# Performance work log

Measured on AMD Instinct MI355X. Metric: run time of the kernel, lower is better.

The kernel has to match this reference:

```python
import jax, jax.numpy as jnp
import numpy as np

HIDDEN = 1024
FFN = 2048
NUM_EXPERTS = 16
JITTER_EPS = 0.01


def setup_inputs() -> dict:
    key = jax.random.key(0)
    k1, k2, k3, k4 = jax.random.split(key, 4)
    hidden_states = jax.random.normal(k1, (4, 2048, HIDDEN), dtype=jnp.float32)
    gate_weight = jax.random.normal(k2, (NUM_EXPERTS, HIDDEN), dtype=jnp.float32) * 0.02
    # gate_up_weights[e, :FFN] = w1 (gate proj), [FFN:] = w3 (up proj)
    gate_up_weights = jax.random.normal(k3, (NUM_EXPERTS, 2 * FFN, HIDDEN), dtype=jnp.float32) * 0.02
    down_weights = jax.random.normal(k4, (NUM_EXPERTS, HIDDEN, FFN), dtype=jnp.float32) * 0.02
    return {
        'hidden_states': hidden_states,
        'gate_weight': gate_weight,
        'gate_up_weights': gate_up_weights,
        'down_weights': down_weights,
    }


def sparsemixer(scores, jitter_eps):
    # top-1 selection with jitter mask
    m1 = jnp.max(scores, axis=-1, keepdims=True)              # [T,1]
    ind1 = jnp.argmax(scores, axis=-1, keepdims=True)         # [T,1]
    factor1 = jnp.maximum(jnp.abs(scores), m1)
    mask1 = (m1 - scores) / factor1 > 2.0 * jitter_eps
    gates1 = jax.nn.softmax(jnp.where(mask1, -jnp.inf, scores), axis=-1)
    w1 = jnp.take_along_axis(gates1, ind1, axis=-1)           # [T,1]

    # mask out top-1, select top-2
    top1_onehot = jax.nn.one_hot(ind1[:, 0], scores.shape[-1], dtype=bool)
    masked_scores = jnp.where(top1_onehot, -jnp.inf, scores)
    m2 = jnp.max(masked_scores, axis=-1, keepdims=True)
    ind2 = jnp.argmax(masked_scores, axis=-1, keepdims=True)
    factor2 = jnp.maximum(jnp.abs(scores), m2)
    mask2 = (m2 - scores) / factor2 > 2.0 * jitter_eps
    gates2 = jax.nn.softmax(jnp.where(mask2, -jnp.inf, masked_scores), axis=-1)
    w2 = jnp.take_along_axis(gates2, ind2, axis=-1)           # [T,1]

    multipliers = jnp.concatenate([w1, w2], axis=-1)          # [T,2]
    experts = jnp.concatenate([ind1, ind2], axis=-1)          # [T,2] int
    return multipliers, experts


def fused_moe(x, gate_up_weights, down_weights, routing_weights, selected_experts):
    # x: [T,H], gate_up: [E,2F,H], down: [E,H,F]
    E = gate_up_weights.shape[0]
    ffn = down_weights.shape[2]
    # combine[t,e] = sum_k routing_weights[t,k] * (selected[t,k]==e)
    onehot = jax.nn.one_hot(selected_experts, E, dtype=x.dtype)     # [T,2,E]
    combine = jnp.einsum('tk,tke->te', routing_weights, onehot)     # [T,E]
    out = jnp.zeros_like(x)
    for e in range(E):
        gu = x @ gate_up_weights[e].T                                # [T,2F]
        h = jax.nn.silu(gu[:, :ffn]) * gu[:, ffn:]                   # [T,F]
        out = out + combine[:, e:e + 1] * (h @ down_weights[e].T)    # [T,H]
    return out


def reference(hidden_states, gate_weight, gate_up_weights, down_weights):
    B, S, H = hidden_states.shape
    x = hidden_states.reshape(-1, H)                         # [T,H]
    router_logits = x @ gate_weight.T                        # [T,E]
    routing_weights, selected_experts = sparsemixer(router_logits, JITTER_EPS)
    out = fused_moe(x, gate_up_weights, down_weights, routing_weights, selected_experts)
    return out.reshape(B, S, H), router_logits
```

## Files before the change

kernel.cpp:

```cpp
#include <hip/hip_runtime.h>
#include <hip/hip_bf16.h>
#include <math.h>

#define T_TOKENS 8192
#define HID 1024
#define FFN 2048
#define NEXP 16
#define NPAIR (2*T_TOKENS)
#define TM 128
#define MAXTILES 144

typedef short bf16x8 __attribute__((ext_vector_type(8)));
typedef float f32x4 __attribute__((ext_vector_type(4)));

static const size_t HPACK_OFF = 0;
static const size_t HPACK_SZ  = (size_t)MAXTILES * 32 * 16384;
static const size_t GPACK_OFF = HPACK_OFF + HPACK_SZ;
static const size_t GPACK_SZ  = (size_t)16 * 64 * 16 * 8192;
static const size_t DPACK_OFF = GPACK_OFF + GPACK_SZ;
static const size_t DPACK_SZ  = (size_t)16 * 16 * 32 * 8192;
static const size_t APACK_OFF = DPACK_OFF + DPACK_SZ;
static const size_t APACK_SZ  = (size_t)MAXTILES * 16 * 16384;
static const size_t WTK_OFF   = APACK_OFF + APACK_SZ;
static const size_t ETK_OFF   = WTK_OFF  + (size_t)NPAIR*4;
static const size_t RANK_OFF  = ETK_OFF  + (size_t)NPAIR*4;
static const size_t LIST_OFF  = RANK_OFF + (size_t)NPAIR*4;
static const size_t CNT_OFF   = LIST_OFF + (size_t)NPAIR*4;
static const size_t OFFS_OFF  = CNT_OFF  + 64;
static const size_t TEXP_OFF  = OFFS_OFF + 128;
static const size_t TSEG_OFF  = TEXP_OFF + (size_t)MAXTILES*4;
static const size_t HDR_OFF   = TSEG_OFF + (size_t)MAXTILES*4;

__device__ __forceinline__ unsigned short f2bf(float f) {
  union { float f; unsigned u; } v; v.f = f;
  unsigned r = v.u + 0x7fff + ((v.u >> 16) & 1);
  return (unsigned short)(r >> 16);
}

__device__ __forceinline__ bf16x8 pack8(float4 a, float4 b) {
  bf16x8 r;
  r[0]=(short)f2bf(a.x); r[1]=(short)f2bf(a.y); r[2]=(short)f2bf(a.z); r[3]=(short)f2bf(a.w);
  r[4]=(short)f2bf(b.x); r[5]=(short)f2bf(b.y); r[6]=(short)f2bf(b.z); r[7]=(short)f2bf(b.w);
  return r;
}

__device__ __forceinline__ void ld16(const unsigned short* g, unsigned short* l) {
  __builtin_amdgcn_global_load_lds((const __attribute__((address_space(1))) void*)g,
                                   (__attribute__((address_space(3))) void*)l, 16, 0, 0);
}

__global__ __launch_bounds__(256) void k_pack(const float* __restrict__ src, unsigned short* __restrict__ dst,
                                              int nbcnt, int kbcnt, int kdim) {
  int e = blockIdx.z, nb = blockIdx.y, kb = blockIdx.x;
  __shared__ unsigned short tile[4096];
  int tid = threadIdx.x;
  int n = tid >> 2, ks = (tid & 3) * 16;
  const float* s = src + ((size_t)((e*nbcnt + nb)*64 + n))*kdim + kb*64 + ks;
  float4 f0 = *(const float4*)(s);
  float4 f1 = *(const float4*)(s + 4);
  float4 f2 = *(const float4*)(s + 8);
  float4 f3 = *(const float4*)(s + 12);
  int kkc0 = ks >> 3;
  *(bf16x8*)&tile[(kkc0*64 + n)*8]     = pack8(f0, f1);
  *(bf16x8*)&tile[((kkc0+1)*64 + n)*8] = pack8(f2, f3);
  __syncthreads();
  unsigned short* d = dst + ((size_t)(e*nbcnt + nb)*kbcnt + kb)*4096 + tid*16;
  *(bf16x8*)(d)     = *(const bf16x8*)&tile[tid*16];
  *(bf16x8*)(d + 8) = *(const bf16x8*)&tile[tid*16 + 8];
}

__global__ __launch_bounds__(256) void k_logits(const float* __restrict__ x,
                                                const float* __restrict__ gw,
                                                float* __restrict__ logits) {
  int tid = threadIdx.x;
  int wave = tid >> 6, lane = tid & 63;
  int t = blockIdx.x * 4 + wave;
  const float* xp = x + (size_t)t * HID;
  float acc[NEXP];
  #pragma unroll
  for (int e = 0; e < NEXP; e++) acc[e] = 0.f;
  for (int i = lane; i < HID; i += 64) {
    float xv = xp[i];
    #pragma unroll
    for (int e = 0; e < NEXP; e++) acc[e] += xv * gw[e*HID + i];
  }
  float mine = 0.f;
  #pragma unroll
  for (int e = 0; e < NEXP; e++) {
    float v = acc[e];
    #pragma unroll
    for (int o = 32; o > 0; o >>= 1) v += __shfl_xor(v, o, 64);
    if (lane == e) mine = v;
  }
  if (lane < NEXP) logits[(size_t)t*NEXP + lane] = mine;
}

__global__ __launch_bounds__(256) void k_route(const float* __restrict__ logits,
                                               float* __restrict__ wtk, int* __restrict__ etk,
                                               int* __restrict__ rank, int* __restrict__ counts) {
  int t = blockIdx.x*256 + threadIdx.x;
  if (t >= T_TOKENS) return;
  float s[NEXP];
  const float* lp = logits + (size_t)t*NEXP;
  #pragma unroll
  for (int e = 0; e < NEXP; e++) s[e] = lp[e];

  float m1 = s[0]; int i1 = 0;
  #pragma unroll
  for (int e = 1; e < NEXP; e++) if (s[e] > m1) { m1 = s[e]; i1 = e; }
  float sum1 = 0.f;
  #pragma unroll
  for (int e = 0; e < NEXP; e++) {
    float f = fmaxf(fabsf(s[e]), m1);
    if (!((m1 - s[e]) > 0.02f*f)) sum1 += expf(s[e]-m1);
  }
  float m2 = -INFINITY; int i2 = 0;
  #pragma unroll
  for (int e = 0; e < NEXP; e++) if (e != i1 && s[e] > m2) { m2 = s[e]; i2 = e; }
  float sum2 = 0.f;
  #pragma unroll
  for (int e = 0; e < NEXP; e++) {
    if (e == i1) continue;
    float f = fmaxf(fabsf(s[e]), m2);
    if (!((m2 - s[e]) > 0.02f*f)) sum2 += expf(s[e]-m2);
  }
  wtk[t*2]   = 1.f/sum1;
  wtk[t*2+1] = 1.f/sum2;
  etk[t*2]   = i1;
  etk[t*2+1] = i2;
  rank[t*2]   = atomicAdd(&counts[i1], 1);
  rank[t*2+1] = atomicAdd(&counts[i2], 1);
}

__global__ void k_scan(const int* __restrict__ counts, int* __restrict__ offsets,
                       int* __restrict__ texp, int* __restrict__ tseg, int* __restrict__ hdr) {
  if (threadIdx.x != 0 || blockIdx.x != 0) return;
  int off = 0, nt = 0;
  for (int e = 0; e < NEXP; e++) {
    offsets[e] = off;
    int c = counts[e];
    int tiles = (c + TM - 1)/TM;
    for (int i = 0; i < tiles; i++) { texp[nt] = e; tseg[nt] = i; nt++; }
    off += c;
  }
  offsets[NEXP] = off;
  hdr[0] = nt;
}

__global__ __launch_bounds__(256) void k_scatter(const int* __restrict__ etk,
                                                 const int* __restrict__ rank,
                                                 const int* __restrict__ offsets,
                                                 int* __restrict__ list) {
  int p = blockIdx.x*256 + threadIdx.x;
  if (p >= NPAIR) return;
  int e = etk[p];
  list[offsets[e] + rank[p]] = p;
}

__global__ __launch_bounds__(256) void k_agather(const float* __restrict__ x,
                                                 const int* __restrict__ list,
                                                 const int* __restrict__ counts,
                                                 const int* __restrict__ offsets,
                                                 const int* __restrict__ texp,
                                                 const int* __restrict__ tseg,
                                                 const int* __restrict__ hdr,
                                                 unsigned short* __restrict__ apack) {
  int by = blockIdx.x;
  if (by >= hdr[0]) return;
  int e = texp[by];
  int m0 = tseg[by]*TM;
  int seg0 = offsets[e];
  int cnt = counts[e];
  __shared__ int toks[TM];
  int tid = threadIdx.x;
  if (tid < TM) toks[tid] = list[seg0 + min(m0 + tid, cnt-1)] >> 1;
  __syncthreads();
  #pragma unroll 4
  for (int it = 0; it < 64; ++it) {
    int flat = it*256 + tid;
    int kb = flat >> 10;
    int i  = flat & 1023;
    int kkc = i >> 7, row = i & 127;
    const float* s = x + (size_t)toks[row]*HID + kb*64 + kkc*8;
    float4 f0 = *(const float4*)(s);
    float4 f1 = *(const float4*)(s + 4);
    *(bf16x8*)(apack + ((size_t)(by*16 + kb))*8192 + (size_t)i*8) = pack8(f0, f1);
  }
}

__global__ __launch_bounds__(256,4) void k_gateup(const unsigned short* __restrict__ apack,
                                                  const unsigned short* __restrict__ gpack,
                                                  const float* __restrict__ wtk,
                                                  const int* __restrict__ list,
                                                  const int* __restrict__ counts,
                                                  const int* __restrict__ offsets,
                                                  const int* __restrict__ texp,
                                                  const int* __restrict__ tseg,
                                                  const int* __restrict__ hdr,
                                                  unsigned short* __restrict__ hpack) {
  int fb = blockIdx.x;
  int by = blockIdx.y;
  if (by >= hdr[0]) return;
  int e = texp[by];
  int m0 = tseg[by]*TM;
  int seg0 = offsets[e];
  int cnt = counts[e];
  int rows = min(TM, cnt - m0);

  __shared__ __align__(16) unsigned short A_lds[8192];
  __shared__ __align__(16) unsigned short Bg_lds[4096];
  __shared__ __align__(16) unsigned short Bu_lds[4096];

  int tid = threadIdx.x;
  int wid = tid >> 6, lane = tid & 63;
  int wr = wid >> 1, wc = wid & 1;
  int c4 = lane >> 4, r16 = lane & 15;

  const unsigned short* gA = apack + (size_t)by * 16 * 8192;
  const unsigned short* gG = gpack + (size_t)(e*64 + fb)      * 16 * 4096;
  const unsigned short* gU = gpack + (size_t)(e*64 + 32 + fb) * 16 * 4096;

  f32x4 accg[4][2] = {};
  f32x4 accu[4][2] = {};

  for (int kb = 0; kb < 16; ++kb) {
    #pragma unroll
    for (int s = 0; s < 8; ++s) {
      int i = wid*8 + s;
      if (i < 16) {
        ld16(gA + (size_t)kb*8192 + i*512 + lane*8, &A_lds[i*512]);
      } else if (i < 24) {
        int j = i - 16;
        ld16(gG + (size_t)kb*4096 + j*512 + lane*8, &Bg_lds[j*512]);
      } else {
        int j = i - 24;
        ld16(gU + (size_t)kb*4096 + j*512 + lane*8, &Bu_lds[j*512]);
      }
    }
    __syncthreads();
    #pragma unroll
    for (int kk = 0; kk < 2; ++kk) {
      bf16x8 a[4], bg[2], bu[2];
      #pragma unroll
      for (int sm = 0; sm < 4; ++sm)
        a[sm] = *(const bf16x8*)&A_lds[((kk*4 + c4)*128 + wr*64 + sm*16 + r16)*8];
      #pragma unroll
      for (int sn = 0; sn < 2; ++sn) {
        bg[sn] = *(const bf16x8*)&Bg_lds[((kk*4 + c4)*64 + wc*32 + sn*16 + r16)*8];
        bu[sn] = *(const bf16x8*)&Bu_lds[((kk*4 + c4)*64 + wc*32 + sn*16 + r16)*8];
      }
      #pragma unroll
      for (int sm = 0; sm < 4; ++sm)
        #pragma unroll
        for (int sn = 0; sn < 2; ++sn) {
          accg[sm][sn] = __builtin_amdgcn_mfma_f32_16x16x32_bf16(a[sm], bg[sn], accg[sm][sn], 0, 0, 0);
          accu[sm][sn] = __builtin_amdgcn_mfma_f32_16x16x32_bf16(a[sm], bu[sn], accu[sm][sn], 0, 0, 0);
        }
    }
    __syncthreads();
  }

  #pragma unroll
  for (int sm = 0; sm < 4; ++sm) {
    #pragma unroll
    for (int j = 0; j < 4; ++j) {
      int row = wr*64 + sm*16 + (lane>>4)*4 + j;
      float w = (row < rows) ? wtk[list[seg0 + m0 + row]] : 0.f;
      #pragma unroll
      for (int sn = 0; sn < 2; ++sn) {
        int col = wc*32 + sn*16 + (lane & 15);
        float g = accg[sm][sn][j];
        float u = accu[sm][sn][j];
        float hv = g / (1.f + __expf(-g)) * u * w;
        A_lds[((col>>3)*128 + row)*8 + (col&7)] = f2bf(hv);
      }
    }
  }
  __syncthreads();
  unsigned short* dst = hpack + ((size_t)(by*32 + fb))*8192 + tid*32;
  const unsigned short* srcl = &A_lds[tid*32];
  #pragma unroll
  for (int q = 0; q < 4; ++q)
    *(bf16x8*)(dst + q*8) = *(const bf16x8*)(srcl + q*8);
}

__global__ __launch_bounds__(256,4) void k_down(const unsigned short* __restrict__ hpack,
                                                const unsigned short* __restrict__ dpack,
                                                const int* __restrict__ list,
                                                const int* __restrict__ counts,
                                                const int* __restrict__ offsets,
                                                const int* __restrict__ texp,
                                                const int* __restrict__ tseg,
                                                const int* __restrict__ hdr,
                                                float* __restrict__ out) {
  int nb = blockIdx.x;
  int by = blockIdx.y;
  if (by >= hdr[0]) return;
  int e = texp[by];
  int m0 = tseg[by]*TM;
  int seg0 = offsets[e];
  int cnt = counts[e];
  int rows = min(TM, cnt - m0);

  __shared__ __align__(16) unsigned short A_lds[8192];
  __shared__ __align__(16) unsigned short B_lds[8192];

  int tid = threadIdx.x;
  int wid = tid >> 6, lane = tid & 63;
  int wr = wid >> 1, wc = wid & 1;
  int c4 = lane >> 4, r16 = lane & 15;

  const unsigned short* hA = hpack + (size_t)by * 32 * 8192;

  f32x4 acc[4][4] = {};

  for (int kb = 0; kb < 32; ++kb) {
    #pragma unroll
    for (int s = 0; s < 8; ++s) {
      int i = wid*8 + s;
      if (i < 16) {
        ld16(hA + (size_t)kb*8192 + i*512 + lane*8, &A_lds[i*512]);
      } else {
        int i2 = i - 16;
        int p = i2 >> 3, j = i2 & 7;
        ld16(dpack + (((size_t)(e*16 + nb*2 + p))*32 + kb)*4096 + j*512 + lane*8,
             &B_lds[p*4096 + j*512]);
      }
    }
    __syncthreads();
    #pragma unroll
    for (int kk = 0; kk < 2; ++kk) {
      bf16x8 a[4], b[4];
      #pragma unroll
      for (int sm = 0; sm < 4; ++sm)
        a[sm] = *(const bf16x8*)&A_lds[((kk*4 + c4)*128 + wr*64 + sm*16 + r16)*8];
      #pragma unroll
      for (int sn = 0; sn < 4; ++sn) {
        int col = wc*64 + sn*16 + r16;
        b[sn] = *(const bf16x8*)&B_lds[(col>>6)*4096 + ((kk*4 + c4)*64 + (col & 63))*8];
      }
      #pragma unroll
      for (int sm = 0; sm < 4; ++sm)
        #pragma unroll
        for (int sn = 0; sn < 4; ++sn)
          acc[sm][sn] = __builtin_amdgcn_mfma_f32_16x16x32_bf16(a[sm], b[sn], acc[sm][sn], 0, 0, 0);
    }
    __syncthreads();
  }

  #pragma unroll
  for (int sm = 0; sm < 4; ++sm) {
    #pragma unroll
    for (int j = 0; j < 4; ++j) {
      int row = wr*64 + sm*16 + (lane>>4)*4 + j;
      if (row < rows) {
        int t = list[seg0 + m0 + row] >> 1;
        #pragma unroll
        for (int sn = 0; sn < 4; ++sn) {
          int col = nb*128 + wc*64 + sn*16 + r16;
          unsafeAtomicAdd(&out[(size_t)t*HID + col], acc[sm][sn][j]);
        }
      }
    }
  }
}

extern "C" void kernel_launch(void* const* d_in, const int* in_sizes, int n_in,
                              void* d_out, int out_size, void* d_ws, size_t ws_size,
                              hipStream_t stream) {
  const float* x   = (const float*)d_in[0];
  const float* gw  = (const float*)d_in[1];
  const float* gup = (const float*)d_in[2];
  const float* dwn = (const float*)d_in[3];

  float* out = (float*)d_out;
  float* logits = out + (size_t)T_TOKENS*HID;

  char* ws = (char*)d_ws;
  unsigned short* hpack = (unsigned short*)(ws + HPACK_OFF);
  unsigned short* gpack = (unsigned short*)(ws + GPACK_OFF);
  unsigned short* dpack = (unsigned short*)(ws + DPACK_OFF);
  unsigned short* apack = (unsigned short*)(ws + APACK_OFF);
  float* wtk   = (float*)(ws + WTK_OFF);
  int* etk     = (int*)(ws + ETK_OFF);
  int* rank    = (int*)(ws + RANK_OFF);
  int* list    = (int*)(ws + LIST_OFF);
  int* counts  = (int*)(ws + CNT_OFF);
  int* offsets = (int*)(ws + OFFS_OFF);
  int* texp    = (int*)(ws + TEXP_OFF);
  int* tseg    = (int*)(ws + TSEG_OFF);
  int* hdr     = (int*)(ws + HDR_OFF);

  hipMemsetAsync(out, 0, (size_t)T_TOKENS*HID*4, stream);
  hipMemsetAsync(counts, 0, 64, stream);

  k_logits<<<T_TOKENS/4, 256, 0, stream>>>(x, gw, logits);
  k_route<<<T_TOKENS/256, 256, 0, stream>>>(logits, wtk, etk, rank, counts);
  k_scan<<<1, 64, 0, stream>>>(counts, offsets, texp, tseg, hdr);
  k_scatter<<<NPAIR/256, 256, 0, stream>>>(etk, rank, offsets, list);
  k_agather<<<MAXTILES, 256, 0, stream>>>(x, list, counts, offsets, texp, tseg, hdr, apack);

  {
    dim3 g(16, 64, NEXP);
    k_pack<<<g, 256, 0, stream>>>(gup, gpack, 64, 16, HID);
  }
  {
    dim3 g(32, 16, NEXP);
    k_pack<<<g, 256, 0, stream>>>(dwn, dpack, 16, 32, FFN);
  }

  dim3 g3(32, MAXTILES);
  k_gateup<<<g3, 256, 0, stream>>>(apack, gpack, wtk, list, counts, offsets, texp, tseg, hdr, hpack);

  dim3 g4(8, MAXTILES);
  k_down<<<g4, 256, 0, stream>>>(hpack, dpack, list, counts, offsets, texp, tseg, hdr, out);
}
```

Measured before the change: 569.5 us.

## Double-buffer LDS in expert GEMMs and replace atomic scatter with slot buffer plus combine

The gate-up and down GEMM kernels now load half-size K tiles into ping-pong LDS buffers, so the global-to-LDS copy for the next step is issued before the MFMAs on the current one. The down kernel no longer atomically adds into the output. It writes each routed row into a per-slot buffer that reuses the gpack workspace region, and a new k_final kernel sums each token's two slots into the output, which also removes the output memset. This trades atomics and the memset for one extra kernel launch and an extra write-then-read of a 64 MB intermediate.

```diff
diff --git a/kernel.cpp b/kernel.cpp
--- a/kernel.cpp
+++ b/kernel.cpp
@@ -207,59 +207,70 @@
   int cnt = counts[e];
   int rows = min(TM, cnt - m0);
 
-  __shared__ __align__(16) unsigned short A_lds[8192];
-  __shared__ __align__(16) unsigned short Bg_lds[4096];
-  __shared__ __align__(16) unsigned short Bu_lds[4096];
+  __shared__ __align__(16) unsigned short A_lds[2][4096];
+  __shared__ __align__(16) unsigned short Bg_lds[2][2048];
+  __shared__ __align__(16) unsigned short Bu_lds[2][2048];
 
   int tid = threadIdx.x;
   int wid = tid >> 6, lane = tid & 63;
   int wr = wid >> 1, wc = wid & 1;
   int c4 = lane >> 4, r16 = lane & 15;
 
-  const unsigned short* gA = apack + (size_t)by * 16 * 8192;
-  const unsigned short* gG = gpack + (size_t)(e*64 + fb)      * 16 * 4096;
-  const unsigned short* gU = gpack + (size_t)(e*64 + 32 + fb) * 16 * 4096;
+  const unsigned short* gA = apack + (size_t)by * 131072;
+  const unsigned short* gG = gpack + ((size_t)(e*64 + fb))      * 65536;
+  const unsigned short* gU = gpack + ((size_t)(e*64 + 32 + fb)) * 65536;
 
   f32x4 accg[4][2] = {};
   f32x4 accu[4][2] = {};
 
-  for (int kb = 0; kb < 16; ++kb) {
-    #pragma unroll
-    for (int s = 0; s < 8; ++s) {
-      int i = wid*8 + s;
-      if (i < 16) {
-        ld16(gA + (size_t)kb*8192 + i*512 + lane*8, &A_lds[i*512]);
-      } else if (i < 24) {
-        int j = i - 16;
-        ld16(gG + (size_t)kb*4096 + j*512 + lane*8, &Bg_lds[j*512]);
+  auto STAGE = [&](int buf, int kb) {
+    #pragma unroll
+    for (int s = 0; s < 4; ++s) {
+      int i = wid*4 + s;
+      if (i < 8) {
+        ld16(gA + (size_t)kb*4096 + i*512 + lane*8, &A_lds[buf][i*512]);
+      } else if (i < 12) {
+        int j = i - 8;
+        ld16(gG + (size_t)kb*2048 + j*512 + lane*8, &Bg_lds[buf][j*512]);
       } else {
-        int j = i - 24;
-        ld16(gU + (size_t)kb*4096 + j*512 + lane*8, &Bu_lds[j*512]);
+        int j = i - 12;
+        ld16(gU + (size_t)kb*2048 + j*512 + lane*8, &Bu_lds[buf][j*512]);
       }
     }
-    __syncthreads();
-    #pragma unroll
-    for (int kk = 0; kk < 2; ++kk) {
-      bf16x8 a[4], bg[2], bu[2];
-      #pragma unroll
-      for (int sm = 0; sm < 4; ++sm)
-        a[sm] = *(const bf16x8*)&A_lds[((kk*4 + c4)*128 + wr*64 + sm*16 + r16)*8];
+  };
+
+  auto COMPUTE = [&](int buf) {
+    bf16x8 a[4], bg[2], bu[2];
+    #pragma unroll
+    for (int sm = 0; sm < 4; ++sm)
+      a[sm] = *(const bf16x8*)&A_lds[buf][(c4*128 + wr*64 + sm*16 + r16)*8];
+    #pragma unroll
+    for (int sn = 0; sn < 2; ++sn) {
+      bg[sn] = *(const bf16x8*)&Bg_lds[buf][(c4*64 + wc*32 + sn*16 + r16)*8];
+      bu[sn] = *(const bf16x8*)&Bu_lds[buf][(c4*64 + wc*32 + sn*16 + r16)*8];
+    }
+    #pragma unroll
+    for (int sm = 0; sm < 4; ++sm)
       #pragma unroll
       for (int sn = 0; sn < 2; ++sn) {
-        bg[sn] = *(const bf16x8*)&Bg_lds[((kk*4 + c4)*64 + wc*32 + sn*16 + r16)*8];
-        bu[sn] = *(const bf16x8*)&Bu_lds[((kk*4 + c4)*64 + wc*32 + sn*16 + r16)*8];
+        accg[sm][sn] = __builtin_amdgcn_mfma_f32_16x16x32_bf16(a[sm], bg[sn], accg[sm][sn], 0, 0, 0);
+        accu[sm][sn] = __builtin_amdgcn_mfma_f32_16x16x32_bf16(a[sm], bu[sn], accu[sm][sn], 0, 0, 0);
       }
-      #pragma unroll
-      for (int sm = 0; sm < 4; ++sm)
-        #pragma unroll
-        for (int sn = 0; sn < 2; ++sn) {
-          accg[sm][sn] = __builtin_amdgcn_mfma_f32_16x16x32_bf16(a[sm], bg[sn], accg[sm][sn], 0, 0, 0);
-          accu[sm][sn] = __builtin_amdgcn_mfma_f32_16x16x32_bf16(a[sm], bu[sn], accu[sm][sn], 0, 0, 0);
-        }
-    }
+  };
+
+  STAGE(0, 0);
+  __syncthreads();
+  int cur = 0;
+  for (int kb = 0; kb < 31; ++kb) {
+    STAGE(cur ^ 1, kb + 1);
+    COMPUTE(cur);
     __syncthreads();
-  }
-
+    cur ^= 1;
+  }
+  COMPUTE(cur);
+  __syncthreads();
+
+  unsigned short* scr = &A_lds[0][0];
   #pragma unroll
   for (int sm = 0; sm < 4; ++sm) {
     #pragma unroll
@@ -272,13 +283,13 @@
         float g = accg[sm][sn][j];
         float u = accu[sm][sn][j];
         float hv = g / (1.f + __expf(-g)) * u * w;
-        A_lds[((col>>3)*128 + row)*8 + (col&7)] = f2bf(hv);
+        scr[((col>>3)*128 + row)*8 + (col&7)] = f2bf(hv);
       }
     }
   }
   __syncthreads();
   unsigned short* dst = hpack + ((size_t)(by*32 + fb))*8192 + tid*32;
-  const unsigned short* srcl = &A_lds[tid*32];
+  const unsigned short* srcl = scr + tid*32;
   #pragma unroll
   for (int q = 0; q < 4; ++q)
     *(bf16x8*)(dst + q*8) = *(const bf16x8*)(srcl + q*8);
@@ -286,13 +297,12 @@
 
 __global__ __launch_bounds__(256,4) void k_down(const unsigned short* __restrict__ hpack,
                                                 const unsigned short* __restrict__ dpack,
-                                                const int* __restrict__ list,
                                                 const int* __restrict__ counts,
-                                                const int* __restrict__ offsets,
                                                 const int* __restrict__ texp,
                                                 const int* __restrict__ tseg,
+                                                const int* __restrict__ offsets,
                                                 const int* __restrict__ hdr,
-                                                float* __restrict__ out) {
+                                                float* __restrict__ ydown) {
   int nb = blockIdx.x;
   int by = blockIdx.y;
   if (by >= hdr[0]) return;
@@ -302,51 +312,60 @@
   int cnt = counts[e];
   int rows = min(TM, cnt - m0);
 
-  __shared__ __align__(16) unsigned short A_lds[8192];
-  __shared__ __align__(16) unsigned short B_lds[8192];
+  __shared__ __align__(16) unsigned short A_lds[2][4096];
+  __shared__ __align__(16) unsigned short B_lds[2][4096];
 
   int tid = threadIdx.x;
   int wid = tid >> 6, lane = tid & 63;
   int wr = wid >> 1, wc = wid & 1;
   int c4 = lane >> 4, r16 = lane & 15;
 
-  const unsigned short* hA = hpack + (size_t)by * 32 * 8192;
+  const unsigned short* hA = hpack + (size_t)by * 262144;
 
   f32x4 acc[4][4] = {};
 
-  for (int kb = 0; kb < 32; ++kb) {
-    #pragma unroll
-    for (int s = 0; s < 8; ++s) {
-      int i = wid*8 + s;
-      if (i < 16) {
-        ld16(hA + (size_t)kb*8192 + i*512 + lane*8, &A_lds[i*512]);
+  auto STAGE = [&](int buf, int kb) {
+    #pragma unroll
+    for (int s = 0; s < 4; ++s) {
+      int i = wid*4 + s;
+      if (i < 8) {
+        ld16(hA + (size_t)kb*4096 + i*512 + lane*8, &A_lds[buf][i*512]);
       } else {
-        int i2 = i - 16;
-        int p = i2 >> 3, j = i2 & 7;
-        ld16(dpack + (((size_t)(e*16 + nb*2 + p))*32 + kb)*4096 + j*512 + lane*8,
-             &B_lds[p*4096 + j*512]);
+        int i2 = i - 8;
+        int p = i2 >> 2, j = i2 & 3;
+        ld16(dpack + (((size_t)(e*16 + nb*2 + p))*32 + (kb>>1))*4096 + (kb&1)*2048 + j*512 + lane*8,
+             &B_lds[buf][p*2048 + j*512]);
       }
     }
+  };
+
+  auto COMPUTE = [&](int buf) {
+    bf16x8 a[4], b[4];
+    #pragma unroll
+    for (int sm = 0; sm < 4; ++sm)
+      a[sm] = *(const bf16x8*)&A_lds[buf][(c4*128 + wr*64 + sm*16 + r16)*8];
+    #pragma unroll
+    for (int sn = 0; sn < 4; ++sn) {
+      int col = wc*64 + sn*16 + r16;
+      b[sn] = *(const bf16x8*)&B_lds[buf][(col>>6)*2048 + (c4*64 + (col&63))*8];
+    }
+    #pragma unroll
+    for (int sm = 0; sm < 4; ++sm)
+      #pragma unroll
+      for (int sn = 0; sn < 4; ++sn)
+        acc[sm][sn] = __builtin_amdgcn_mfma_f32_16x16x32_bf16(a[sm], b[sn], acc[sm][sn], 0, 0, 0);
+  };
+
+  STAGE(0, 0);
+  __syncthreads();
+  int cur = 0;
+  for (int kb = 0; kb < 63; ++kb) {
+    STAGE(cur ^ 1, kb + 1);
+    COMPUTE(cur);
     __syncthreads();
-    #pragma unroll
-    for (int kk = 0; kk < 2; ++kk) {
-      bf16x8 a[4], b[4];
-      #pragma unroll
-      for (int sm = 0; sm < 4; ++sm)
-        a[sm] = *(const bf16x8*)&A_lds[((kk*4 + c4)*128 + wr*64 + sm*16 + r16)*8];
-      #pragma unroll
-      for (int sn = 0; sn < 4; ++sn) {
-        int col = wc*64 + sn*16 + r16;
-        b[sn] = *(const bf16x8*)&B_lds[(col>>6)*4096 + ((kk*4 + c4)*64 + (col & 63))*8];
-      }
-      #pragma unroll
-      for (int sm = 0; sm < 4; ++sm)
-        #pragma unroll
-        for (int sn = 0; sn < 4; ++sn)
-          acc[sm][sn] = __builtin_amdgcn_mfma_f32_16x16x32_bf16(a[sm], b[sn], acc[sm][sn], 0, 0, 0);
-    }
-    __syncthreads();
-  }
+    cur ^= 1;
+  }
+  COMPUTE(cur);
 
   #pragma unroll
   for (int sm = 0; sm < 4; ++sm) {
@@ -354,15 +373,31 @@
     for (int j = 0; j < 4; ++j) {
       int row = wr*64 + sm*16 + (lane>>4)*4 + j;
       if (row < rows) {
-        int t = list[seg0 + m0 + row] >> 1;
+        size_t slot = (size_t)(seg0 + m0 + row);
         #pragma unroll
         for (int sn = 0; sn < 4; ++sn) {
           int col = nb*128 + wc*64 + sn*16 + r16;
-          unsafeAtomicAdd(&out[(size_t)t*HID + col], acc[sm][sn][j]);
+          ydown[slot*HID + col] = acc[sm][sn][j];
         }
       }
     }
   }
+}
+
+__global__ __launch_bounds__(256) void k_final(const float* __restrict__ ydown,
+                                               const int* __restrict__ etk,
+                                               const int* __restrict__ rank,
+                                               const int* __restrict__ offsets,
+                                               float* __restrict__ out) {
+  int t = blockIdx.x;
+  int c = threadIdx.x;
+  int p0 = t*2, p1 = t*2 + 1;
+  int s0 = offsets[etk[p0]] + rank[p0];
+  int s1 = offsets[etk[p1]] + rank[p1];
+  float4 a = *(const float4*)(ydown + (size_t)s0*HID + c*4);
+  float4 b = *(const float4*)(ydown + (size_t)s1*HID + c*4);
+  float4 r; r.x = a.x+b.x; r.y = a.y+b.y; r.z = a.z+b.z; r.w = a.w+b.w;
+  *(float4*)(out + (size_t)t*HID + c*4) = r;
 }
 
 extern "C" void kernel_launch(void* const* d_in, const int* in_sizes, int n_in,
@@ -381,6 +416,7 @@
   unsigned short* gpack = (unsigned short*)(ws + GPACK_OFF);
   unsigned short* dpack = (unsigned short*)(ws + DPACK_OFF);
   unsigned short* apack = (unsigned short*)(ws + APACK_OFF);
+  float* ydown = (float*)(ws + GPACK_OFF);
   float* wtk   = (float*)(ws + WTK_OFF);
   int* etk     = (int*)(ws + ETK_OFF);
   int* rank    = (int*)(ws + RANK_OFF);
@@ -391,7 +427,6 @@
   int* tseg    = (int*)(ws + TSEG_OFF);
   int* hdr     = (int*)(ws + HDR_OFF);
 
-  hipMemsetAsync(out, 0, (size_t)T_TOKENS*HID*4, stream);
   hipMemsetAsync(counts, 0, 64, stream);
 
   k_logits<<<T_TOKENS/4, 256, 0, stream>>>(x, gw, logits);
@@ -413,5 +448,7 @@
   k_gateup<<<g3, 256, 0, stream>>>(apack, gpack, wtk, list, counts, offsets, texp, tseg, hdr, hpack);
 
   dim3 g4(8, MAXTILES);
-  k_down<<<g4, 256, 0, stream>>>(hpack, dpack, list, counts, offsets, texp, tseg, hdr, out);
-}
+  k_down<<<g4, 256, 0, stream>>>(hpack, dpack, counts, texp, tseg, offsets, hdr, ydown);
+
+  k_final<<<T_TOKENS, 256, 0, stream>>>(ydown, etk, rank, offsets, out);
+}
```

Result: no change. 562.8 us (-1.2%).

## Merge pack kernels into gather/gate-up launches and replace atomics with slot-ordered reduction

Applied to the files above, without the earlier changes.

The gate-up weight pack now runs inside the token-gather launch, and the down-weight pack runs as extra blocks of the gate-up launch, which cuts the launch count and lets the packing overlap with other work. The down projection no longer does atomic adds into a zeroed output. It writes each pair's result to a per-slot buffer that reuses the gate-pack workspace, and a new final kernel sums the two expert contributions per token. This removes the output memset and the atomic contention, at the cost of an extra 64MB write and read. Reusing gpack space for ydown is only safe because gate-up has finished by the time down runs.

```diff
diff --git a/kernel.cpp b/kernel.cpp
--- a/kernel.cpp
+++ b/kernel.cpp
@@ -49,10 +49,9 @@
                                    (__attribute__((address_space(3))) void*)l, 16, 0, 0);
 }
 
-__global__ __launch_bounds__(256) void k_pack(const float* __restrict__ src, unsigned short* __restrict__ dst,
-                                              int nbcnt, int kbcnt, int kdim) {
-  int e = blockIdx.z, nb = blockIdx.y, kb = blockIdx.x;
-  __shared__ unsigned short tile[4096];
+__device__ __forceinline__ void pack_body(const float* __restrict__ src, unsigned short* __restrict__ dst,
+                                          int e, int nb, int kb, int nbcnt, int kbcnt, int kdim,
+                                          unsigned short* tile ) {
   int tid = threadIdx.x;
   int n = tid >> 2, ks = (tid & 3) * 16;
   const float* s = src + ((size_t)((e*nbcnt + nb)*64 + n))*kdim + kb*64 + ks;
@@ -157,21 +156,30 @@
   list[offsets[e] + rank[p]] = p;
 }
 
-__global__ __launch_bounds__(256) void k_agather(const float* __restrict__ x,
-                                                 const int* __restrict__ list,
-                                                 const int* __restrict__ counts,
-                                                 const int* __restrict__ offsets,
-                                                 const int* __restrict__ texp,
-                                                 const int* __restrict__ tseg,
-                                                 const int* __restrict__ hdr,
-                                                 unsigned short* __restrict__ apack) {
-  int by = blockIdx.x;
+__global__ __launch_bounds__(256) void k_prep(const float* __restrict__ gup,
+                                              unsigned short* __restrict__ gpack,
+                                              const float* __restrict__ x,
+                                              const int* __restrict__ list,
+                                              const int* __restrict__ counts,
+                                              const int* __restrict__ offsets,
+                                              const int* __restrict__ texp,
+                                              const int* __restrict__ tseg,
+                                              const int* __restrict__ hdr,
+                                              unsigned short* __restrict__ apack) {
+  __shared__ __align__(16) unsigned short tile[4096];
+  int bid = blockIdx.x;
+  if (bid < 16384) {
+    int kb = bid & 15, nb = (bid >> 4) & 63, e = bid >> 10;
+    pack_body(gup, gpack, e, nb, kb, 64, 16, HID, tile);
+    return;
+  }
+  int by = bid - 16384;
   if (by >= hdr[0]) return;
   int e = texp[by];
   int m0 = tseg[by]*TM;
   int seg0 = offsets[e];
   int cnt = counts[e];
-  __shared__ int toks[TM];
+  int* toks = (int*)tile;
   int tid = threadIdx.x;
   if (tid < TM) toks[tid] = list[seg0 + min(m0 + tid, cnt-1)] >> 1;
   __syncthreads();
@@ -190,6 +198,8 @@
 
 __global__ __launch_bounds__(256,4) void k_gateup(const unsigned short* __restrict__ apack,
                                                   const unsigned short* __restrict__ gpack,
+                                                  const float* __restrict__ dwn,
+                                                  unsigned short* __restrict__ dpack,
                                                   const float* __restrict__ wtk,
                                                   const int* __restrict__ list,
                                                   const int* __restrict__ counts,
@@ -198,8 +208,15 @@
                                                   const int* __restrict__ tseg,
                                                   const int* __restrict__ hdr,
                                                   unsigned short* __restrict__ hpack) {
-  int fb = blockIdx.x;
-  int by = blockIdx.y;
+  __shared__ __align__(16) unsigned short lds[16384];
+  int bid = blockIdx.x;
+  if (bid >= 4608) {
+    int p = bid - 4608;
+    pack_body(dwn, dpack, p >> 9, (p >> 5) & 15, p & 31, 16, 32, FFN, lds);
+    return;
+  }
+  int fb = bid & 31;
+  int by = bid >> 5;
   if (by >= hdr[0]) return;
   int e = texp[by];
   int m0 = tseg[by]*TM;
@@ -207,18 +224,18 @@
   int cnt = counts[e];
   int rows = min(TM, cnt - m0);
 
-  __shared__ __align__(16) unsigned short A_lds[8192];
-  __shared__ __align__(16) unsigned short Bg_lds[4096];
-  __shared__ __align__(16) unsigned short Bu_lds[4096];
+  unsigned short* A_lds  = lds;
+  unsigned short* Bg_lds = lds + 8192;
+  unsigned short* Bu_lds = lds + 12288;
 
   int tid = threadIdx.x;
   int wid = tid >> 6, lane = tid & 63;
   int wr = wid >> 1, wc = wid & 1;
   int c4 = lane >> 4, r16 = lane & 15;
 
-  const unsigned short* gA = apack + (size_t)by * 16 * 8192;
-  const unsigned short* gG = gpack + (size_t)(e*64 + fb)      * 16 * 4096;
-  const unsigned short* gU = gpack + (size_t)(e*64 + 32 + fb) * 16 * 4096;
+  const unsigned short* gA = apack + (size_t)by * 131072;
+  const unsigned short* gG = gpack + (size_t)(e*64 + fb)      * 65536;
+  const unsigned short* gU = gpack + (size_t)(e*64 + 32 + fb) * 65536;
 
   f32x4 accg[4][2] = {};
   f32x4 accu[4][2] = {};
@@ -286,13 +303,12 @@
 
 __global__ __launch_bounds__(256,4) void k_down(const unsigned short* __restrict__ hpack,
                                                 const unsigned short* __restrict__ dpack,
-                                                const int* __restrict__ list,
                                                 const int* __restrict__ counts,
-                                                const int* __restrict__ offsets,
                                                 const int* __restrict__ texp,
                                                 const int* __restrict__ tseg,
+                                                const int* __restrict__ offsets,
                                                 const int* __restrict__ hdr,
-                                                float* __restrict__ out) {
+                                                float* __restrict__ ydown) {
   int nb = blockIdx.x;
   int by = blockIdx.y;
   if (by >= hdr[0]) return;
@@ -310,7 +326,7 @@
   int wr = wid >> 1, wc = wid & 1;
   int c4 = lane >> 4, r16 = lane & 15;
 
-  const unsigned short* hA = hpack + (size_t)by * 32 * 8192;
+  const unsigned short* hA = hpack + (size_t)by * 262144;
 
   f32x4 acc[4][4] = {};
 
@@ -354,15 +370,31 @@
     for (int j = 0; j < 4; ++j) {
       int row = wr*64 + sm*16 + (lane>>4)*4 + j;
       if (row < rows) {
-        int t = list[seg0 + m0 + row] >> 1;
+        size_t slot = (size_t)(seg0 + m0 + row);
         #pragma unroll
         for (int sn = 0; sn < 4; ++sn) {
           int col = nb*128 + wc*64 + sn*16 + r16;
-          unsafeAtomicAdd(&out[(size_t)t*HID + col], acc[sm][sn][j]);
+          ydown[slot*HID + col] = acc[sm][sn][j];
         }
       }
     }
   }
+}
+
+__global__ __launch_bounds__(256) void k_final(const float* __restrict__ ydown,
+                                               const int* __restrict__ etk,
+                                               const int* __restrict__ rank,
+                                               const int* __restrict__ offsets,
+                                               float* __restrict__ out) {
+  int t = blockIdx.x;
+  int c = threadIdx.x;
+  int p0 = t*2, p1 = t*2 + 1;
+  int s0 = offsets[etk[p0]] + rank[p0];
+  int s1 = offsets[etk[p1]] + rank[p1];
+  float4 a = *(const float4*)(ydown + (size_t)s0*HID + c*4);
+  float4 b = *(const float4*)(ydown + (size_t)s1*HID + c*4);
+  float4 r; r.x = a.x+b.x; r.y = a.y+b.y; r.z = a.z+b.z; r.w = a.w+b.w;
+  *(float4*)(out + (size_t)t*HID + c*4) = r;
 }
 
 extern "C" void kernel_launch(void* const* d_in, const int* in_sizes, int n_in,
@@ -381,6 +413,7 @@
   unsigned short* gpack = (unsigned short*)(ws + GPACK_OFF);
   unsigned short* dpack = (unsigned short*)(ws + DPACK_OFF);
   unsigned short* apack = (unsigned short*)(ws + APACK_OFF);
+  float* ydown = (float*)(ws + GPACK_OFF);
   float* wtk   = (float*)(ws + WTK_OFF);
   int* etk     = (int*)(ws + ETK_OFF);
   int* rank    = (int*)(ws + RANK_OFF);
@@ -391,27 +424,20 @@
   int* tseg    = (int*)(ws + TSEG_OFF);
   int* hdr     = (int*)(ws + HDR_OFF);
 
-  hipMemsetAsync(out, 0, (size_t)T_TOKENS*HID*4, stream);
   hipMemsetAsync(counts, 0, 64, stream);
 
   k_logits<<<T_TOKENS/4, 256, 0, stream>>>(x, gw, logits);
   k_route<<<T_TOKENS/256, 256, 0, stream>>>(logits, wtk, etk, rank, counts);
   k_scan<<<1, 64, 0, stream>>>(counts, offsets, texp, tseg, hdr);
   k_scatter<<<NPAIR/256, 256, 0, stream>>>(etk, rank, offsets, list);
-  k_agather<<<MAXTILES, 256, 0, stream>>>(x, list, counts, offsets, texp, tseg, hdr, apack);
-
-  {
-    dim3 g(16, 64, NEXP);
-    k_pack<<<g, 256, 0, stream>>>(gup, gpack, 64, 16, HID);
-  }
-  {
-    dim3 g(32, 16, NEXP);
-    k_pack<<<g, 256, 0, stream>>>(dwn, dpack, 16, 32, FFN);
-  }
-
-  dim3 g3(32, MAXTILES);
-  k_gateup<<<g3, 256, 0, stream>>>(apack, gpack, wtk, list, counts, offsets, texp, tseg, hdr, hpack);
+
+  k_prep<<<16384 + MAXTILES, 256, 0, stream>>>(gup, gpack, x, list, counts, offsets, texp, tseg, hdr, apack);
+
+  k_gateup<<<4608 + 8192, 256, 0, stream>>>(apack, gpack, dwn, dpack, wtk, list, counts, offsets,
+                                            texp, tseg, hdr, hpack);
 
   dim3 g4(8, MAXTILES);
-  k_down<<<g4, 256, 0, stream>>>(hpack, dpack, list, counts, offsets, texp, tseg, hdr, out);
-}
+  k_down<<<g4, 256, 0, stream>>>(hpack, dpack, counts, texp, tseg, offsets, hdr, ydown);
+
+  k_final<<<T_TOKENS, 256, 0, stream>>>(ydown, etk, rank, offsets, out);
+}
```

After: 528.5 us. 7.2% less time.
